# Kernel tuning notes

Measured on AMD Instinct MI355X. Metric: run time of the kernel, lower is better.

Reference implementation:

```python
import jax, jax.numpy as jnp
import numpy as np

DIM, DK, DV = 1024, 128, 128
B, S = 4, 2048

def setup_inputs() -> dict:
    key = jax.random.key(0)
    ks = jax.random.split(key, 7)
    s = lambda d: 1.0 / np.sqrt(d)
    return {
        "x":  jax.random.normal(ks[0], (B, S, DIM), dtype=jnp.float32),
        "Wq": jax.random.normal(ks[1], (DIM, DK), dtype=jnp.float32) * s(DIM),
        "bq": jax.random.normal(ks[2], (DK,), dtype=jnp.float32) * 0.02,
        "Wk": jax.random.normal(ks[3], (DIM, DK), dtype=jnp.float32) * s(DIM),
        "bk": jax.random.normal(ks[4], (DK,), dtype=jnp.float32) * 0.02,
        "Wv": jax.random.normal(ks[5], (DIM, DV), dtype=jnp.float32) * s(DIM),
        "bv": jax.random.normal(ks[6], (DV,), dtype=jnp.float32) * 0.02,
    }

def reference(x, Wq, bq, Wk, bk, Wv, bv):
    scale = DK ** (-0.5)
    q = x @ Wq + bq                      # [B,S,DK]
    k = x @ Wk + bk                      # [B,S,DK]
    v = x @ Wv + bv                      # [B,S,DV]
    attn = jnp.einsum('bsd,btd->bst', q, k) * scale  # [B,S,S]
    attn = jax.nn.softmax(attn, axis=-1)
    return jnp.einsum('bst,btd->bsd', attn, v)       # [B,S,DV]
```

## Files before the change

kernel.cpp:

```cpp
#include <hip/hip_runtime.h>

typedef unsigned short u16;
typedef unsigned int u32;
typedef __bf16 bf16;
typedef __bf16 bf16x8 __attribute__((ext_vector_type(8)));
typedef float f32x4 __attribute__((ext_vector_type(4)));
typedef u32 u32x4 __attribute__((ext_vector_type(4)));


__device__ __forceinline__ void gl_lds16(const void* g, void* l) {
  __builtin_amdgcn_global_load_lds(
      (const __attribute__((address_space(1))) void*)g,
      (__attribute__((address_space(3))) void*)l, 16, 0, 0);
}
__device__ __forceinline__ u16 bfbits(float f) {
  return __builtin_bit_cast(u16, (bf16)f);
}
__device__ __forceinline__ u32 pk2(float lo, float hi) {
  return (u32)bfbits(lo) | ((u32)bfbits(hi) << 16);
}
__device__ __forceinline__ float fexp2(float x) {
  return __builtin_amdgcn_exp2f(x);
}

__global__ __launch_bounds__(256) void wprep_kernel(
    const float* __restrict__ Wq, const float* __restrict__ Wk,
    const float* __restrict__ Wv, u16* __restrict__ Wt) {
  __shared__ u16 st[64][72];
  const int tid = threadIdx.x;
  const int m = blockIdx.x >> 5, rem = blockIdx.x & 31, kt = rem >> 1, nt = rem & 1;
  const float* W = (m == 0) ? Wq : (m == 1) ? Wk : Wv;
  const int k0 = kt * 64, n0 = nt * 64;
#pragma unroll
  for (int i = 0; i < 4; ++i) {
    int kk = i * 16 + (tid >> 4), nn = (tid & 15) * 4;
    f32x4 w = *(const f32x4*)&W[(size_t)(k0 + kk) * 128 + n0 + nn];
    st[kk][nn]     = bfbits(w[0]); st[kk][nn + 1] = bfbits(w[1]);
    st[kk][nn + 2] = bfbits(w[2]); st[kk][nn + 3] = bfbits(w[3]);
  }
  __syncthreads();
#pragma unroll
  for (int i = 0; i < 4; ++i) {
    int nn = i * 16 + (tid >> 4), kk = (tid & 15) * 4;
    ushort4 u;
    u.x = st[kk][nn]; u.y = st[kk + 1][nn]; u.z = st[kk + 2][nn]; u.w = st[kk + 3][nn];
    *(ushort4*)&Wt[(size_t)m * 131072 + (size_t)(n0 + nn) * 1024 + k0 + kk] = u;
  }
}

__global__ __launch_bounds__(256) void qkv_gemm(
    const float* __restrict__ x, const u16* __restrict__ Wt,
    const float* __restrict__ bq, const float* __restrict__ bk, const float* __restrict__ bv,
    u16* __restrict__ qb, u16* __restrict__ kb, u16* __restrict__ vt)
{
  __shared__ __attribute__((aligned(16))) u16 sxb[2][64 * 64];
  __shared__ __attribute__((aligned(16))) u16 sw[2][128 * 64];
  const int tid = threadIdx.x, wid = tid >> 6, lane = tid & 63;
  const int g = lane >> 4, q16 = lane & 15;
  const int m = blockIdx.y;
  const int row0 = blockIdx.x * 64;
  const u16* W = Wt + (size_t)m * 131072;
  const int wr = wid >> 1, wc = wid & 1;

  const float* xsrc[2]; int xdo[2];
#pragma unroll
  for (int i = 0; i < 2; ++i) {
    int fc = i * 256 + tid, r = fc >> 3, c = fc & 7;
    xsrc[i] = x + (size_t)(row0 + r) * 1024 + c * 8;
    xdo[i] = r * 64 + ((c ^ (r & 7)) << 3);
  }

  f32x4 xst[2][2];
  auto XLOAD = [&](int k0) {
#pragma unroll
    for (int i = 0; i < 2; ++i) {
      xst[i][0] = *(const f32x4*)(xsrc[i] + k0);
      xst[i][1] = *(const f32x4*)(xsrc[i] + k0 + 4);
    }
  };
  auto XWRITE = [&](int buf) {
#pragma unroll
    for (int i = 0; i < 2; ++i) {
      u32x4 v = {pk2(xst[i][0][0], xst[i][0][1]), pk2(xst[i][0][2], xst[i][0][3]),
                 pk2(xst[i][1][0], xst[i][1][1]), pk2(xst[i][1][2], xst[i][1][3])};
      *(u32x4*)&sxb[buf][xdo[i]] = v;
    }
  };
  auto WSTAGE = [&](int buf, int k0) {
#pragma unroll
    for (int i = 0; i < 4; ++i) {
      int fc = i * 256 + tid; int r = fc >> 3, c = fc & 7;
      gl_lds16(W + (size_t)r * 1024 + k0 + ((c ^ (r & 7)) << 3),
               (char*)&sw[buf][0] + fc * 16);
    }
  };

  f32x4 acc[2][4] = {};
  XLOAD(0); WSTAGE(0, 0);
  asm volatile("s_waitcnt vmcnt(0)" ::: "memory");
  XWRITE(0);
  __syncthreads();
  int cur = 0;

  for (int kt = 0; kt < 16; ++kt) {
    if (kt < 15) { XLOAD((kt + 1) * 64); WSTAGE(cur ^ 1, (kt + 1) * 64); }
    const u16* sxc = &sxb[cur][0];
    const u16* swc = &sw[cur][0];
#pragma unroll
    for (int ks = 0; ks < 2; ++ks) {
      bf16x8 af[2], bfr[4];
#pragma unroll
      for (int mr = 0; mr < 2; ++mr) {
        int row = wr * 32 + mr * 16 + q16;
        int ch = (ks * 4 + g) ^ (row & 7);
        af[mr] = *(const bf16x8*)(sxc + row * 64 + ch * 8);
      }
#pragma unroll
      for (int nr = 0; nr < 4; ++nr) {
        int row = wc * 64 + nr * 16 + q16;
        int ch = (ks * 4 + g) ^ (row & 7);
        bfr[nr] = *(const bf16x8*)(swc + row * 64 + ch * 8);
      }
#pragma unroll
      for (int mr = 0; mr < 2; ++mr)
#pragma unroll
        for (int nr = 0; nr < 4; ++nr)
          acc[mr][nr] = __builtin_amdgcn_mfma_f32_16x16x32_bf16(af[mr], bfr[nr], acc[mr][nr], 0, 0, 0);
    }
    if (kt < 15) {
      asm volatile("s_waitcnt vmcnt(0)" ::: "memory");
      XWRITE(cur ^ 1);
      __syncthreads();
      cur ^= 1;
    }
  }

  const float* bias = (m == 0) ? bq : (m == 1) ? bk : bv;
  u16* qk = (m == 0) ? qb : kb;
#pragma unroll
  for (int mr = 0; mr < 2; ++mr) {
#pragma unroll
    for (int nr = 0; nr < 4; ++nr) {
      int col = wc * 64 + nr * 16 + q16;
      float bc = bias[col];
      int grow = row0 + wr * 32 + mr * 16 + g * 4;
      if (m == 2) {
        int bb = grow >> 11;
        int sbase = ((grow & 2047) & ~31) | (g * 8 + mr * 4);
        ushort4 u;
        u.x = bfbits(acc[mr][nr][0] + bc);
        u.y = bfbits(acc[mr][nr][1] + bc);
        u.z = bfbits(acc[mr][nr][2] + bc);
        u.w = bfbits(acc[mr][nr][3] + bc);
        *(ushort4*)&vt[(size_t)bb * 262144 + (size_t)col * 2048 + sbase] = u;
      } else {
#pragma unroll
        for (int r = 0; r < 4; ++r)
          qk[(size_t)(grow + r) * 128 + col] = bfbits(acc[mr][nr][r] + bc);
      }
    }
  }
}

union ALDS {
  u16 stg[8][8192];
  struct {
    float oc[8][32 * 132];
    float l[8][32];
    float linv[32];
  } cb;
};

__global__ __launch_bounds__(512) void attn_kernel(
    const u16* __restrict__ qb, const u16* __restrict__ kb, const u16* __restrict__ vt,
    float* __restrict__ out)
{
  __shared__ __attribute__((aligned(16))) ALDS lds;
  const int tid = threadIdx.x, wid = tid >> 6, lane = tid & 63;
  const int g = lane >> 4, q16 = lane & 15;
  const int bid = blockIdx.x;
  const int b = (bid & 7) >> 1;
  const int qt = ((bid >> 3) << 1) | (bid & 1);
  const size_t qgA = (size_t)b * 2048 + qt * 32;
  const u16* kbw = kb + ((size_t)b * 2048 + wid * 256) * 128;
  const u16* vbw = vt + (size_t)b * 262144 + wid * 256;
  u16* skw = &lds.stg[wid][0];
  u16* svw = &lds.stg[wid][4096];
  const float scale2 = 0.08838834764831845f * 1.4426950408889634f;

  bf16x8 qfA[4], qfB[4];
#pragma unroll
  for (int kg = 0; kg < 4; ++kg) {
    qfA[kg] = *(const bf16x8*)&qb[(qgA + q16) * 128 + kg * 32 + g * 8];
    qfB[kg] = *(const bf16x8*)&qb[(qgA + 16 + q16) * 128 + kg * 32 + g * 8];
  }

  auto SK = [&](int t) {
#pragma unroll
    for (int i = 0; i < 8; ++i) {
      int fc = i * 64 + lane; int r = fc >> 4, c = fc & 15;
      gl_lds16(kbw + (size_t)(t * 32 + r) * 128 + ((c ^ (r & 7)) << 3),
               (char*)skw + fc * 16);
    }
  };
  auto SV = [&](int t) {
#pragma unroll
    for (int i = 0; i < 8; ++i) {
      int fc = i * 64 + lane; int r = fc >> 2, c = fc & 3;
      int h = (r ^ (r >> 2)) & 3;
      gl_lds16(vbw + (size_t)r * 2048 + t * 32 + ((c ^ h) << 3),
               (char*)svw + fc * 16);
    }
  };

  float lA = 0.f, lB = 0.f;
  f32x4 accA[8] = {}, accB[8] = {};

  SK(0); SV(0);
  for (int t = 0; t < 8; ++t) {
    asm volatile("s_waitcnt vmcnt(8)" ::: "memory");

    f32x4 sTa[2] = {}, sTb[2] = {};
#pragma unroll
    for (int kg = 0; kg < 4; ++kg)
#pragma unroll
      for (int jg = 0; jg < 2; ++jg) {
        int row = jg * 16 + q16;
        int ch = (kg * 4 + g) ^ (row & 7);
        bf16x8 kf = *(const bf16x8*)(skw + row * 128 + ch * 8);
        sTa[jg] = __builtin_amdgcn_mfma_f32_16x16x32_bf16(kf, qfA[kg], sTa[jg], 0, 0, 0);
        sTb[jg] = __builtin_amdgcn_mfma_f32_16x16x32_bf16(kf, qfB[kg], sTb[jg], 0, 0, 0);
      }
    __builtin_amdgcn_sched_barrier(0);
    if (t < 7) SK(t + 1);

    u32 WpA[2][2], WpB[2][2];
#pragma unroll
    for (int jg = 0; jg < 2; ++jg) {
      float e0 = fexp2(sTa[jg][0] * scale2);
      float e1 = fexp2(sTa[jg][1] * scale2);
      float e2 = fexp2(sTa[jg][2] * scale2);
      float e3 = fexp2(sTa[jg][3] * scale2);
      lA += (e0 + e1) + (e2 + e3);
      WpA[jg][0] = pk2(e0, e1);
      WpA[jg][1] = pk2(e2, e3);
    }
#pragma unroll
    for (int jg = 0; jg < 2; ++jg) {
      float e0 = fexp2(sTb[jg][0] * scale2);
      float e1 = fexp2(sTb[jg][1] * scale2);
      float e2 = fexp2(sTb[jg][2] * scale2);
      float e3 = fexp2(sTb[jg][3] * scale2);
      lB += (e0 + e1) + (e2 + e3);
      WpB[jg][0] = pk2(e0, e1);
      WpB[jg][1] = pk2(e2, e3);
    }

    u32x4 wa = {WpA[0][0], WpA[0][1], WpA[1][0], WpA[1][1]};
    u32x4 wb = {WpB[0][0], WpB[0][1], WpB[1][0], WpB[1][1]};
    bf16x8 pA = __builtin_bit_cast(bf16x8, wa);
    bf16x8 pB = __builtin_bit_cast(bf16x8, wb);

    if (t < 7) { asm volatile("s_waitcnt vmcnt(8)" ::: "memory"); }
    else       { asm volatile("s_waitcnt vmcnt(0)" ::: "memory"); }

#pragma unroll
    for (int dg = 0; dg < 8; ++dg) {
      int row = dg * 16 + q16;
      int ch = g ^ ((row ^ (row >> 2)) & 3);
      bf16x8 vf = *(const bf16x8*)(svw + row * 32 + ch * 8);
      accA[dg] = __builtin_amdgcn_mfma_f32_16x16x32_bf16(vf, pA, accA[dg], 0, 0, 0);
      accB[dg] = __builtin_amdgcn_mfma_f32_16x16x32_bf16(vf, pB, accB[dg], 0, 0, 0);
    }
    __builtin_amdgcn_sched_barrier(0);
    if (t < 7) SV(t + 1);
  }

  lA += __shfl_xor(lA, 16); lA += __shfl_xor(lA, 32);
  lB += __shfl_xor(lB, 16); lB += __shfl_xor(lB, 32);

  __syncthreads();
  {
    float* ocp = &lds.cb.oc[wid][0];
#pragma unroll
    for (int dg = 0; dg < 8; ++dg) {
      *(f32x4*)&ocp[q16 * 132 + dg * 16 + g * 4] = accA[dg];
      *(f32x4*)&ocp[(16 + q16) * 132 + dg * 16 + g * 4] = accB[dg];
    }
    if (g == 0) {
      lds.cb.l[wid][q16] = lA;
      lds.cb.l[wid][16 + q16] = lB;
    }
  }
  __syncthreads();
  if (tid < 32) {
    int q = tid;
    float s = 0.f;
#pragma unroll
    for (int w = 0; w < 8; ++w) s += lds.cb.l[w][q];
    lds.cb.linv[q] = 1.0f / s;
  }
  __syncthreads();
#pragma unroll
  for (int h = 0; h < 2; ++h) {
    int idx = h * 512 + tid;
    int q = idx >> 5, d4 = idx & 31;
    f32x4 v = {0.f, 0.f, 0.f, 0.f};
#pragma unroll
    for (int w = 0; w < 8; ++w)
      v += *(const f32x4*)&lds.cb.oc[w][q * 132 + d4 * 4];
    v *= lds.cb.linv[q];
    *(f32x4*)&out[((size_t)b * 2048 + qt * 32 + q) * 128 + d4 * 4] = v;
  }
}

extern "C" void kernel_launch(void* const* d_in, const int* in_sizes, int n_in,
                              void* d_out, int out_size, void* d_ws, size_t ws_size,
                              hipStream_t stream)
{
  (void)in_sizes; (void)n_in; (void)out_size; (void)ws_size;
  const float* x  = (const float*)d_in[0];
  const float* Wq = (const float*)d_in[1];
  const float* bq = (const float*)d_in[2];
  const float* Wk = (const float*)d_in[3];
  const float* bk = (const float*)d_in[4];
  const float* Wv = (const float*)d_in[5];
  const float* bv = (const float*)d_in[6];
  char* ws = (char*)d_ws;
  u16* qbuf  = (u16*)(ws);
  u16* kbuf  = (u16*)(ws + (2u << 20));
  u16* vtbuf = (u16*)(ws + (4u << 20));
  u16* Wt    = (u16*)(ws + (6u << 20));

  wprep_kernel<<<96, 256, 0, stream>>>(Wq, Wk, Wv, Wt);
  qkv_gemm<<<dim3(128, 3), 256, 0, stream>>>(x, Wt, bq, bk, bv, qbuf, kbuf, vtbuf);
  attn_kernel<<<256, 512, 0, stream>>>(qbuf, kbuf, vtbuf, (float*)d_out);
}
```

Baseline: 54.64 us.

## Fuse weight-prep into QKV GEMM with a global atomic flag barrier

The separate weight transpose/convert kernel is folded into the QKV GEMM kernel. The first 96 blocks convert the weights, then signal through an atomic counter, and every block spins on that counter before staging weights. The x load for the first tile is issued before this wait so its latency overlaps. The aim is to drop one kernel launch and its inter-kernel gap. In exchange it adds a memset and relies on all 96 producer blocks being co-resident with the waiting blocks, which could deadlock if they are not.

```diff
diff --git a/kernel.cpp b/kernel.cpp
--- a/kernel.cpp
+++ b/kernel.cpp
@@ -23,42 +23,25 @@
   return __builtin_amdgcn_exp2f(x);
 }
 
-__global__ __launch_bounds__(256) void wprep_kernel(
-    const float* __restrict__ Wq, const float* __restrict__ Wk,
-    const float* __restrict__ Wv, u16* __restrict__ Wt) {
-  __shared__ u16 st[64][72];
-  const int tid = threadIdx.x;
-  const int m = blockIdx.x >> 5, rem = blockIdx.x & 31, kt = rem >> 1, nt = rem & 1;
-  const float* W = (m == 0) ? Wq : (m == 1) ? Wk : Wv;
-  const int k0 = kt * 64, n0 = nt * 64;
-#pragma unroll
-  for (int i = 0; i < 4; ++i) {
-    int kk = i * 16 + (tid >> 4), nn = (tid & 15) * 4;
-    f32x4 w = *(const f32x4*)&W[(size_t)(k0 + kk) * 128 + n0 + nn];
-    st[kk][nn]     = bfbits(w[0]); st[kk][nn + 1] = bfbits(w[1]);
-    st[kk][nn + 2] = bfbits(w[2]); st[kk][nn + 3] = bfbits(w[3]);
-  }
-  __syncthreads();
-#pragma unroll
-  for (int i = 0; i < 4; ++i) {
-    int nn = i * 16 + (tid >> 4), kk = (tid & 15) * 4;
-    ushort4 u;
-    u.x = st[kk][nn]; u.y = st[kk + 1][nn]; u.z = st[kk + 2][nn]; u.w = st[kk + 3][nn];
-    *(ushort4*)&Wt[(size_t)m * 131072 + (size_t)(n0 + nn) * 1024 + k0 + kk] = u;
-  }
-}
-
-__global__ __launch_bounds__(256) void qkv_gemm(
-    const float* __restrict__ x, const u16* __restrict__ Wt,
-    const float* __restrict__ bq, const float* __restrict__ bk, const float* __restrict__ bv,
-    u16* __restrict__ qb, u16* __restrict__ kb, u16* __restrict__ vt)
+union QLDS {
+  u16 st[64 * 72];
+  struct { u16 sxb[2][64 * 64]; u16 sw[2][128 * 64]; } qk;
+};
+
+__global__ __launch_bounds__(256) void qkvw_kernel(
+    const float* __restrict__ x,
+    const float* __restrict__ Wq, const float* __restrict__ bq,
+    const float* __restrict__ Wk, const float* __restrict__ bk,
+    const float* __restrict__ Wv, const float* __restrict__ bv,
+    u16* __restrict__ qb, u16* __restrict__ kb, u16* __restrict__ vt,
+    u16* __restrict__ Wt, u32* __restrict__ flag)
 {
-  __shared__ __attribute__((aligned(16))) u16 sxb[2][64 * 64];
-  __shared__ __attribute__((aligned(16))) u16 sw[2][128 * 64];
+  __shared__ __attribute__((aligned(16))) QLDS lds;
   const int tid = threadIdx.x, wid = tid >> 6, lane = tid & 63;
   const int g = lane >> 4, q16 = lane & 15;
   const int m = blockIdx.y;
   const int row0 = blockIdx.x * 64;
+  const int lid = blockIdx.y * 128 + blockIdx.x;
   const u16* W = Wt + (size_t)m * 131072;
   const int wr = wid >> 1, wc = wid & 1;
 
@@ -83,7 +66,7 @@
     for (int i = 0; i < 2; ++i) {
       u32x4 v = {pk2(xst[i][0][0], xst[i][0][1]), pk2(xst[i][0][2], xst[i][0][3]),
                  pk2(xst[i][1][0], xst[i][1][1]), pk2(xst[i][1][2], xst[i][1][3])};
-      *(u32x4*)&sxb[buf][xdo[i]] = v;
+      *(u32x4*)&lds.qk.sxb[buf][xdo[i]] = v;
     }
   };
   auto WSTAGE = [&](int buf, int k0) {
@@ -91,12 +74,46 @@
     for (int i = 0; i < 4; ++i) {
       int fc = i * 256 + tid; int r = fc >> 3, c = fc & 7;
       gl_lds16(W + (size_t)r * 1024 + k0 + ((c ^ (r & 7)) << 3),
-               (char*)&sw[buf][0] + fc * 16);
-    }
-  };
+               (char*)&lds.qk.sw[buf][0] + fc * 16);
+    }
+  };
+
+  XLOAD(0);
+
+  if (lid < 96) {
+    const int mm = lid >> 5, rem = lid & 31, kt = rem >> 1, nt = rem & 1;
+    const float* Wsrc = (mm == 0) ? Wq : (mm == 1) ? Wk : Wv;
+    const int k0 = kt * 64, n0 = nt * 64;
+#pragma unroll
+    for (int i = 0; i < 4; ++i) {
+      int kk = i * 16 + (tid >> 4), nn = (tid & 15) * 4;
+      f32x4 w = *(const f32x4*)&Wsrc[(size_t)(k0 + kk) * 128 + n0 + nn];
+      lds.st[kk * 72 + nn]     = bfbits(w[0]); lds.st[kk * 72 + nn + 1] = bfbits(w[1]);
+      lds.st[kk * 72 + nn + 2] = bfbits(w[2]); lds.st[kk * 72 + nn + 3] = bfbits(w[3]);
+    }
+    __syncthreads();
+#pragma unroll
+    for (int i = 0; i < 4; ++i) {
+      int nn = i * 16 + (tid >> 4), kk = (tid & 15) * 4;
+      ushort4 u;
+      u.x = lds.st[kk * 72 + nn];       u.y = lds.st[(kk + 1) * 72 + nn];
+      u.z = lds.st[(kk + 2) * 72 + nn]; u.w = lds.st[(kk + 3) * 72 + nn];
+      *(ushort4*)&Wt[(size_t)mm * 131072 + (size_t)(n0 + nn) * 1024 + k0 + kk] = u;
+    }
+  }
+  __syncthreads();
+  if (lid < 96 && tid == 0) {
+    __threadfence();
+    __hip_atomic_fetch_add(flag, 1u, __ATOMIC_ACQ_REL, __HIP_MEMORY_SCOPE_AGENT);
+  }
+  if (tid == 0) {
+    while (__hip_atomic_load(flag, __ATOMIC_ACQUIRE, __HIP_MEMORY_SCOPE_AGENT) < 96u)
+      __builtin_amdgcn_s_sleep(2);
+  }
+  __syncthreads();
 
   f32x4 acc[2][4] = {};
-  XLOAD(0); WSTAGE(0, 0);
+  WSTAGE(0, 0);
   asm volatile("s_waitcnt vmcnt(0)" ::: "memory");
   XWRITE(0);
   __syncthreads();
@@ -104,8 +121,8 @@
 
   for (int kt = 0; kt < 16; ++kt) {
     if (kt < 15) { XLOAD((kt + 1) * 64); WSTAGE(cur ^ 1, (kt + 1) * 64); }
-    const u16* sxc = &sxb[cur][0];
-    const u16* swc = &sw[cur][0];
+    const u16* sxc = &lds.qk.sxb[cur][0];
+    const u16* swc = &lds.qk.sw[cur][0];
 #pragma unroll
     for (int ks = 0; ks < 2; ++ks) {
       bf16x8 af[2], bfr[4];
@@ -331,8 +348,10 @@
   u16* kbuf  = (u16*)(ws + (2u << 20));
   u16* vtbuf = (u16*)(ws + (4u << 20));
   u16* Wt    = (u16*)(ws + (6u << 20));
-
-  wprep_kernel<<<96, 256, 0, stream>>>(Wq, Wk, Wv, Wt);
-  qkv_gemm<<<dim3(128, 3), 256, 0, stream>>>(x, Wt, bq, bk, bv, qbuf, kbuf, vtbuf);
+  u32* flag  = (u32*)(ws + (7u << 20));
+
+  hipMemsetAsync((void*)flag, 0, 256, stream);
+  qkvw_kernel<<<dim3(128, 3), 256, 0, stream>>>(x, Wq, bq, Wk, bk, Wv, bv,
+                                                qbuf, kbuf, vtbuf, Wt, flag);
   attn_kernel<<<256, 512, 0, stream>>>(qbuf, kbuf, vtbuf, (float*)d_out);
 }
```

Measured after the change: 71.71 us. +31.2%, slower.

## Deepen x prefetch in QKV projection to two tiles with partial vmcnt waits

Applied to the files above, without the earlier changes.

The projection GEMM loop is restructured to hold two register buffers for x tiles (A/B), manually unrolled by two. Each x tile is now loaded two k-steps ahead rather than one. The full vmcnt(0) drain is replaced by vmcnt(4), so the latest x load stays in flight while the previous tile is converted to bf16 and written to LDS. The aim is to hide global-load latency of the fp32 x stream behind MFMA work, at the cost of more VGPRs and more complex code.

```diff
diff --git a/kernel.cpp b/kernel.cpp
--- a/kernel.cpp
+++ b/kernel.cpp
@@ -70,22 +70,22 @@
     xdo[i] = r * 64 + ((c ^ (r & 7)) << 3);
   }
 
-  f32x4 xst[2][2];
-  auto XLOAD = [&](int k0) {
-#pragma unroll
-    for (int i = 0; i < 2; ++i) {
-      xst[i][0] = *(const f32x4*)(xsrc[i] + k0);
-      xst[i][1] = *(const f32x4*)(xsrc[i] + k0 + 4);
-    }
-  };
-  auto XWRITE = [&](int buf) {
-#pragma unroll
-    for (int i = 0; i < 2; ++i) {
-      u32x4 v = {pk2(xst[i][0][0], xst[i][0][1]), pk2(xst[i][0][2], xst[i][0][3]),
-                 pk2(xst[i][1][0], xst[i][1][1]), pk2(xst[i][1][2], xst[i][1][3])};
-      *(u32x4*)&sxb[buf][xdo[i]] = v;
-    }
-  };
+  f32x4 xA[2][2], xB[2][2];
+#define XLOAD_A(K0) { _Pragma("unroll") for (int i = 0; i < 2; ++i) { \
+    xA[i][0] = *(const f32x4*)(xsrc[i] + (K0)); \
+    xA[i][1] = *(const f32x4*)(xsrc[i] + (K0) + 4); } }
+#define XLOAD_B(K0) { _Pragma("unroll") for (int i = 0; i < 2; ++i) { \
+    xB[i][0] = *(const f32x4*)(xsrc[i] + (K0)); \
+    xB[i][1] = *(const f32x4*)(xsrc[i] + (K0) + 4); } }
+#define XWRITE_A(BUF) { _Pragma("unroll") for (int i = 0; i < 2; ++i) { \
+    u32x4 v = {pk2(xA[i][0][0], xA[i][0][1]), pk2(xA[i][0][2], xA[i][0][3]), \
+               pk2(xA[i][1][0], xA[i][1][1]), pk2(xA[i][1][2], xA[i][1][3])}; \
+    *(u32x4*)&sxb[BUF][xdo[i]] = v; } }
+#define XWRITE_B(BUF) { _Pragma("unroll") for (int i = 0; i < 2; ++i) { \
+    u32x4 v = {pk2(xB[i][0][0], xB[i][0][1]), pk2(xB[i][0][2], xB[i][0][3]), \
+               pk2(xB[i][1][0], xB[i][1][1]), pk2(xB[i][1][2], xB[i][1][3])}; \
+    *(u32x4*)&sxb[BUF][xdo[i]] = v; } }
+
   auto WSTAGE = [&](int buf, int k0) {
 #pragma unroll
     for (int i = 0; i < 4; ++i) {
@@ -96,16 +96,10 @@
   };
 
   f32x4 acc[2][4] = {};
-  XLOAD(0); WSTAGE(0, 0);
-  asm volatile("s_waitcnt vmcnt(0)" ::: "memory");
-  XWRITE(0);
-  __syncthreads();
-  int cur = 0;
-
-  for (int kt = 0; kt < 16; ++kt) {
-    if (kt < 15) { XLOAD((kt + 1) * 64); WSTAGE(cur ^ 1, (kt + 1) * 64); }
-    const u16* sxc = &sxb[cur][0];
-    const u16* swc = &sw[cur][0];
+
+  auto COMPUTE = [&](int buf) {
+    const u16* sxc = &sxb[buf][0];
+    const u16* swc = &sw[buf][0];
 #pragma unroll
     for (int ks = 0; ks < 2; ++ks) {
       bf16x8 af[2], bfr[4];
@@ -127,13 +121,37 @@
         for (int nr = 0; nr < 4; ++nr)
           acc[mr][nr] = __builtin_amdgcn_mfma_f32_16x16x32_bf16(af[mr], bfr[nr], acc[mr][nr], 0, 0, 0);
     }
-    if (kt < 15) {
-      asm volatile("s_waitcnt vmcnt(0)" ::: "memory");
-      XWRITE(cur ^ 1);
-      __syncthreads();
-      cur ^= 1;
-    }
-  }
+  };
+
+  XLOAD_A(0);
+  WSTAGE(0, 0);
+  XLOAD_B(64);
+  asm volatile("s_waitcnt vmcnt(4)" ::: "memory");
+  XWRITE_A(0);
+  __syncthreads();
+
+#pragma unroll 1
+  for (int kt2 = 0; kt2 < 7; ++kt2) {
+    const int k0 = kt2 * 128;
+    WSTAGE(1, k0 + 64);
+    XLOAD_A(k0 + 128);
+    COMPUTE(0);
+    asm volatile("s_waitcnt vmcnt(4)" ::: "memory");
+    XWRITE_B(1);
+    __syncthreads();
+    WSTAGE(0, k0 + 128);
+    XLOAD_B(k0 + 192);
+    COMPUTE(1);
+    asm volatile("s_waitcnt vmcnt(4)" ::: "memory");
+    XWRITE_A(0);
+    __syncthreads();
+  }
+  WSTAGE(1, 15 * 64);
+  COMPUTE(0);
+  asm volatile("s_waitcnt vmcnt(0)" ::: "memory");
+  XWRITE_B(1);
+  __syncthreads();
+  COMPUTE(1);
 
   const float* bias = (m == 0) ? bq : (m == 1) ? bk : bv;
   u16* qk = (m == 0) ? qb : kb;
@@ -160,6 +178,10 @@
       }
     }
   }
+#undef XLOAD_A
+#undef XLOAD_B
+#undef XWRITE_A
+#undef XWRITE_B
 }
 
 union ALDS {
```

Result: faster. 48.59 us, median of 3 (-11.1%).
